# Performance work log

Hardware: AMD Instinct MI355X
Metric: run time of the kernel (lower is better)

## Reference

```python
import jax, jax.numpy as jnp
import numpy as np

B, T, N, D = 8, 512, 64, 128
PRED, HEADS, HID = 96, 8, 256
KERNELS = (17, 49)
NUM_LAYERS = 1
NUM_BLOCKS = 1
IDX_T = np.arange(64)   # lowest 64 of T//2=256 rfft modes (mode_select='low')
IDX_C = np.arange(32)   # min(modes, (N+1)//2)=32 lowest channel-frequency modes


def _mov_avg(x, k):
    # x: [B, T, N]; replicate-pad (k-1)//2 on both ends, then box filter (AvgPool1d stride 1)
    pad = (k - 1) // 2
    xp = jnp.concatenate([jnp.repeat(x[:, :1], pad, axis=1), x, jnp.repeat(x[:, -1:], pad, axis=1)], axis=1)
    c = jnp.cumsum(xp, axis=1)
    c = jnp.concatenate([jnp.zeros_like(c[:, :1]), c], axis=1)
    return (c[:, k:] - c[:, :-k]) / k


def _decomp_multi(x, dec_w, dec_b):
    # series_decomp_multi: softmax-weighted mixture of moving averages
    mm = jnp.stack([_mov_avg(x, k) for k in KERNELS], axis=-1)        # [B,T,N,K]
    w = jax.nn.softmax(x[..., None] * dec_w + dec_b, axis=-1)         # Linear(1,K) on x, softmax over K
    trend = jnp.sum(mm * w, axis=-1)
    return x - trend, trend


def _complex_attn(x, Wq, Wk, Wv, Wo):
    # x: complex64 [B, L, M, D]; multi-head attention over the M selected frequency modes.
    # Real projection weights applied to complex activations; attention weights are
    # softmax over |q k^H| / sqrt(dh); values stay complex.
    Bq, L, M, Dm = x.shape
    dh = Dm // HEADS
    q = jnp.einsum('blmd,de->blme', x, Wq).reshape(Bq, L, M, HEADS, dh)
    k = jnp.einsum('blmd,de->blme', x, Wk).reshape(Bq, L, M, HEADS, dh)
    v = jnp.einsum('blmd,de->blme', x, Wv).reshape(Bq, L, M, HEADS, dh)
    s = jnp.einsum('blmhd,blnhd->blhmn', q, jnp.conj(k))              # complex scores
    w = jax.nn.softmax(jnp.abs(s) / np.sqrt(dh), axis=-1)             # real attn weights
    o = jnp.einsum('blhmn,blnhd->blmhd', w.astype(x.dtype), v).reshape(Bq, L, M, Dm)
    return jnp.einsum('blmd,de->blme', o, Wo)


def _cem(x, Wq, Wk, Wv, Wo):
    # channel-frequency attention; x: [B, N, T, D]
    xp = jnp.transpose(x, (0, 2, 1, 3))                               # [B,T,N,D]
    xf = jnp.fft.rfft(xp, axis=2)                                     # [B,T,N//2+1,D]
    xs = xf[:, :, IDX_C, :]                                           # gather selected modes
    for _ in range(NUM_LAYERS):
        xs = _complex_attn(xs, Wq, Wk, Wv, Wo)
    yf = jnp.zeros((x.shape[0], T, N // 2 + 1, D), dtype=xf.dtype).at[:, :, IDX_C, :].set(xs)
    y = jnp.fft.irfft(yf, n=N, axis=2)
    return jnp.transpose(y, (0, 2, 1, 3))


def _tem(x, Wq, Wk, Wv, Wo):
    # temporal-frequency attention; x: [B, N, T, D]
    xf = jnp.fft.rfft(x, axis=2)                                      # [B,N,T//2+1,D]
    xs = xf[:, :, IDX_T, :]
    for _ in range(NUM_LAYERS):
        xs = _complex_attn(xs, Wq, Wk, Wv, Wo)
    yf = jnp.zeros((x.shape[0], N, T // 2 + 1, D), dtype=xf.dtype).at[:, :, IDX_T, :].set(xs)
    return jnp.fft.irfft(yf, n=T, axis=2)


def setup_inputs() -> dict:
    key = jax.random.key(0)
    ks = jax.random.split(key, 24)
    r = lambda i, shape, s: jax.random.normal(ks[i], shape, jnp.float32) * s
    K = len(KERNELS)
    return {
        'x': jax.random.normal(ks[0], (B, T, N), jnp.float32),
        'embeddings': jax.random.normal(ks[1], (1, D), jnp.float32),
        'dec_w': r(2, (K,), 1.0),
        'dec_b': jnp.zeros((K,), jnp.float32),
        'mlp_w1': r(3, (T, HID), 1.0 / np.sqrt(T)),
        'mlp_b1': jnp.zeros((HID,), jnp.float32),
        'mlp_w2': r(4, (HID, HID), 1.0 / np.sqrt(HID)),
        'mlp_b2': jnp.zeros((HID,), jnp.float32),
        'mlp_w3': r(5, (HID, PRED), 1.0 / np.sqrt(HID)),
        'mlp_b3': jnp.zeros((PRED,), jnp.float32),
        'cem_Wq': r(6, (D, D), 0.02), 'cem_Wk': r(7, (D, D), 0.02),
        'cem_Wv': r(8, (D, D), 0.02), 'cem_Wo': r(9, (D, D), 0.02),
        'tem_Wq': r(10, (D, D), 0.02), 'tem_Wk': r(11, (D, D), 0.02),
        'tem_Wv': r(12, (D, D), 0.02), 'tem_Wo': r(13, (D, D), 0.02),
        'dr_w': r(14, (D, 1), 1.0 / np.sqrt(D)),
        'dr_b': jnp.zeros((1,), jnp.float32),
        'out_w': r(15, (T, PRED), 1.0 / np.sqrt(T)),
        'out_b': jnp.zeros((PRED,), jnp.float32),
        'W_fuse': jnp.ones((2,), jnp.float32),
    }


def reference(x, embeddings, dec_w, dec_b, mlp_w1, mlp_b1, mlp_w2, mlp_b2, mlp_w3, mlp_b3,
              cem_Wq, cem_Wk, cem_Wv, cem_Wo, tem_Wq, tem_Wk, tem_Wv, tem_Wo,
              dr_w, dr_b, out_w, out_b, W_fuse):
    res, trend = _decomp_multi(x, dec_w, dec_b)
    t = jnp.transpose(trend, (0, 2, 1))                               # [B,N,T]
    h = jax.nn.relu(t @ mlp_w1 + mlp_b1)
    h = jax.nn.relu(h @ mlp_w2 + mlp_b2)
    trend_out = jnp.transpose(h @ mlp_w3 + mlp_b3, (0, 2, 1))         # [B,PRED,N]
    # tokenEmb: [B,T,N] -> [B,N,T,1] * [1,D]
    xe = jnp.transpose(res, (0, 2, 1))[..., None] * embeddings[0]      # [B,N,T,D]
    for _ in range(NUM_BLOCKS):
        xe = _cem(xe, cem_Wq, cem_Wk, cem_Wv, cem_Wo)
    for _ in range(NUM_BLOCKS):
        xe = _tem(xe, tem_Wq, tem_Wk, tem_Wv, tem_Wo)
    xr = jnp.einsum('bntd,do->bnto', xe, dr_w)[..., 0] + dr_b[0]      # dim_reduction -> [B,N,T]
    xo = jnp.transpose(jnp.einsum('bnt,tp->bnp', xr, out_w) + out_b, (0, 2, 1))  # [B,PRED,N]
    return W_fuse[0] * xo + W_fuse[1] * trend_out
```

## Files before the change

### kernel.cpp

```cpp
#include <hip/hip_runtime.h>
#include <hip/hip_bf16.h>

typedef __hip_bfloat16 bf16;

constexpr int CB = 8;
constexpr int CT = 512;
constexpr int CN = 64;
constexpr int CD = 128;
constexpr int CP = 96;
constexpr int CH = 8;
constexpr int CDH = 16;
constexpr int CHID = 256;
constexpr int CM = 32;
constexpr int CG = 64;
constexpr float TWO_PI = 6.28318530717958647692f;

__device__ __forceinline__ float LD(const void* p, size_t i, bool f) {
  return f ? ((const float*)p)[i] : __bfloat162float(((const bf16*)p)[i]);
}
template <bool F32>
__device__ __forceinline__ float LDT(const void* p, size_t i) {
  return F32 ? ((const float*)p)[i] : __bfloat162float(((const bf16*)p)[i]);
}

__device__ __forceinline__ bool detect_f32(const void* x) {
  const unsigned int* xw = (const unsigned int*)x;
  unsigned int w = xw[threadIdx.x & 63];
  unsigned int e = (w >> 7) & 0xFF;
  unsigned long long m = __ballot(e >= 0x90 || e <= 0x60);
  return __popcll(m) > 3;
}

__device__ __forceinline__ float2 pkfma(float2 a, float2 b, float2 c) {
  return make_float2(fmaf(a.x, b.x, c.x), fmaf(a.y, b.y, c.y));
}

struct MArgs {
  const void *x, *dec_w, *dec_b, *out_w, *emb, *cWq, *cWk, *cWv, *cWo;
  const void *tWq, *tWk, *tWv, *tWo, *drw, *drb, *out_b, *wfuse;
  const void *w1, *b1, *w2, *b2, *w3, *b3;
  float *trendo, *Pbuf, *ewq, *ewk, *ewv, *wod, *owr, *owi;
  void* out;
};

template <bool F32>
__device__ void k2_body(float* sm, const MArgs& a) {
  float* xbuf = sm;
  float* rows = sm + 2560;
  float* h1 = sm + 4608;
  float* h2 = sm + 5632;
  int r0 = blockIdx.x * 4;
  int b = r0 >> 6, n0 = r0 & 63;
  int tid = threadIdx.x;
  size_t xb = (size_t)b * CT * CN + n0;
  for (int i = tid; i < CT * 4; i += 256) {
    int t = i >> 2, q = i & 3;
    xbuf[t * 5 + q] = LDT<F32>(a.x, xb + (size_t)t * CN + q);
  }
  __syncthreads();
  {
    float w0 = LDT<F32>(a.dec_w, 0), w1 = LDT<F32>(a.dec_w, 1);
    float c0 = LDT<F32>(a.dec_b, 0), c1 = LDT<F32>(a.dec_b, 1);
    int q = tid & 3, tl = tid >> 2;
    int t0 = tl * 8;
    float s17 = 0.f, s49 = 0.f;
    #pragma unroll
    for (int o = -8; o <= 8; ++o) {
      int u = t0 + o; u = u < 0 ? 0 : (u > CT - 1 ? CT - 1 : u);
      s17 += xbuf[u * 5 + q];
    }
    #pragma unroll
    for (int o = -24; o <= 24; ++o) {
      int u = t0 + o; u = u < 0 ? 0 : (u > CT - 1 ? CT - 1 : u);
      s49 += xbuf[u * 5 + q];
    }
    #pragma unroll
    for (int k = 0; k < 8; ++k) {
      int t = t0 + k;
      if (k > 0) {
        int up8 = t + 8 > CT - 1 ? CT - 1 : t + 8;
        int dn9 = t - 9 < 0 ? 0 : t - 9;
        int up24 = t + 24 > CT - 1 ? CT - 1 : t + 24;
        int dn25 = t - 25 < 0 ? 0 : t - 25;
        s17 += xbuf[up8 * 5 + q] - xbuf[dn9 * 5 + q];
        s49 += xbuf[up24 * 5 + q] - xbuf[dn25 * 5 + q];
      }
      float m0 = s17 * (1.f / 17.f), m1 = s49 * (1.f / 49.f);
      float xv = xbuf[t * 5 + q];
      float l0 = xv * w0 + c0, l1 = xv * w1 + c1;
      float mx = fmaxf(l0, l1);
      float e0 = __expf(l0 - mx), e1 = __expf(l1 - mx);
      rows[q * CT + t] = (e0 * m0 + e1 * m1) / (e0 + e1);
    }
  }
  __syncthreads();
  int c = tid;
  float a0, a1, a2, a3;
  {
    float bias = LDT<F32>(a.b1, c);
    a0 = a1 = a2 = a3 = 0.f;
    #pragma unroll 16
    for (int t = 0; t < CT; ++t) {
      float w = LDT<F32>(a.w1, t * CHID + c);
      a0 += rows[0 * CT + t] * w; a1 += rows[1 * CT + t] * w;
      a2 += rows[2 * CT + t] * w; a3 += rows[3 * CT + t] * w;
    }
    h1[0 * CHID + c] = fmaxf(a0 + bias, 0.f); h1[1 * CHID + c] = fmaxf(a1 + bias, 0.f);
    h1[2 * CHID + c] = fmaxf(a2 + bias, 0.f); h1[3 * CHID + c] = fmaxf(a3 + bias, 0.f);
  }
  __syncthreads();
  {
    float bias = LDT<F32>(a.b2, c);
    a0 = a1 = a2 = a3 = 0.f;
    #pragma unroll 16
    for (int i = 0; i < CHID; ++i) {
      float w = LDT<F32>(a.w2, i * CHID + c);
      a0 += h1[0 * CHID + i] * w; a1 += h1[1 * CHID + i] * w;
      a2 += h1[2 * CHID + i] * w; a3 += h1[3 * CHID + i] * w;
    }
    h2[0 * CHID + c] = fmaxf(a0 + bias, 0.f); h2[1 * CHID + c] = fmaxf(a1 + bias, 0.f);
    h2[2 * CHID + c] = fmaxf(a2 + bias, 0.f); h2[3 * CHID + c] = fmaxf(a3 + bias, 0.f);
  }
  __syncthreads();
  if (tid < 2 * CP) {
    int p = tid < CP ? tid : tid - CP;
    int qh = tid < CP ? 0 : 2;
    float bias = LDT<F32>(a.b3, p);
    a0 = a1 = 0.f;
    #pragma unroll 16
    for (int i = 0; i < CHID; ++i) {
      float w = LDT<F32>(a.w3, i * CP + p);
      a0 += h2[qh * CHID + i] * w; a1 += h2[(qh + 1) * CHID + i] * w;
    }
    a.trendo[((size_t)(b * CN + n0 + qh)) * CP + p] = a0 + bias;
    a.trendo[((size_t)(b * CN + n0 + qh + 1)) * CP + p] = a1 + bias;
  }
}

__global__ __launch_bounds__(256, 4) void kS2(MArgs a) {
  __shared__ __align__(16) float sm[6656];
  bool f32 = detect_f32(a.x);
  int blk = blockIdx.x, tid = threadIdx.x;
  if (blk < 128) {
    if (f32) k2_body<true>(sm, a);
    else     k2_body<false>(sm, a);
  } else if (blk < 1152) {
    float* xl = sm;
    float* rowl = sm + 3328;
    float* Rr = sm + 3584;
    float* Ri = sm + 3712;
    float* aR = sm + 3840;
    float* Sr = sm + 3968;
    float* Si = sm + 4992;
    float* chtmp = sm + 6016;
    float* chl = sm + 6144;
    float* eml = sm + 6152;
    int bk = blk - 128;
    int b = bk >> 7, tbase = (bk & 127) * 4;
    int w = tid >> 6, lane = tid & 63;
    size_t xb = (size_t)b * CT * CN;
    for (int i = tid; i < 52 * 64; i += 256) {
      int r = i >> 6, n = i & 63;
      int u = tbase - 24 + r; u = u < 0 ? 0 : (u > CT - 1 ? CT - 1 : u);
      xl[i] = LD(a.x, xb + (size_t)u * CN + n, f32);
    }
    if (tid < 128) eml[tid] = LD(a.emb, tid, f32);
    __syncthreads();
    if (tid < 128) {
      float pq = 0, pk = 0;
      #pragma unroll 8
      for (int d = 0; d < CD; ++d) {
        float em = eml[d];
        pq += em * LD(a.cWq, d * CD + tid, f32);
        pk += em * LD(a.cWk, d * CD + tid, f32);
      }
      chtmp[tid] = pq * pk;
    }
    __syncthreads();
    if (tid < CH) {
      float s = 0;
      #pragma unroll
      for (int j = 0; j < 16; ++j) s += chtmp[tid * 16 + j];
      chl[tid] = fabsf(s);
    }
    {
      int t = tbase + w;
      int Lt = 24 + w;
      float w0 = LD(a.dec_w, 0, f32), w1 = LD(a.dec_w, 1, f32);
      float c0 = LD(a.dec_b, 0, f32), c1 = LD(a.dec_b, 1, f32);
      float s17 = 0;
      #pragma unroll
      for (int o = -8; o <= 8; ++o) s17 += xl[(Lt + o) * 64 + lane];
      float s49 = 0;
      #pragma unroll
      for (int o = -24; o <= 24; ++o) s49 += xl[(Lt + o) * 64 + lane];
      float m0 = s17 * (1.f / 17.f), m1 = s49 * (1.f / 49.f);
      float xv = xl[Lt * 64 + lane];
      float l0 = xv * w0 + c0, l1 = xv * w1 + c1;
      float mx = fmaxf(l0, l1);
      float e0 = __expf(l0 - mx), e1 = __expf(l1 - mx);
      float tr = (e0 * m0 + e1 * m1) / (e0 + e1);
      rowl[w * 64 + lane] = xv - tr;
      (void)t;
    }
    __syncthreads();
    if (lane < CM) {
      float cf, sf;
      sincosf((float)lane * (TWO_PI / CN), &sf, &cf);
      float wr = 1.f, wi = 0.f, rr = 0.f, ri = 0.f;
      #pragma unroll 8
      for (int n2 = 0; n2 < CN; ++n2) {
        float xv = rowl[w * 64 + n2];
        rr = fmaf(xv, wr, rr); ri = fmaf(-xv, wi, ri);
        float nr = wr * cf - wi * sf; wi = wi * cf + wr * sf; wr = nr;
      }
      Rr[w * 32 + lane] = rr; Ri[w * 32 + lane] = ri;
      aR[w * 32 + lane] = sqrtf(rr * rr + ri * ri);
    }
    __syncthreads();
    float amax = 0;
    for (int m = 0; m < CM; ++m) amax = fmaxf(amax, aR[w * 32 + m]);
    #pragma unroll
    for (int i = 0; i < 4; ++i) {
      int pair = lane + 64 * i;
      int h = pair >> 5, m = pair & 31;
      float alpha = 0.25f * chl[h] * aR[w * 32 + m];
      float den = 0, sr = 0, si = 0;
      for (int n2 = 0; n2 < CM; ++n2) {
        float e = __expf(alpha * (aR[w * 32 + n2] - amax));
        den += e; sr += e * Rr[w * 32 + n2]; si += e * Ri[w * 32 + n2];
      }
      Sr[w * 256 + pair] = sr / den; Si[w * 256 + pair] = si / den;
    }
    __syncthreads();
    {
      int n2 = lane, t = tbase + w;
      float acc[8];
      #pragma unroll
      for (int h = 0; h < CH; ++h) acc[h] = Sr[w * 256 + h * 32];
      float cd, sd;
      sincosf((float)n2 * (TWO_PI / CN), &sd, &cd);
      float px = cd, py = sd;
      for (int f = 1; f < CM; ++f) {
        #pragma unroll
        for (int h = 0; h < CH; ++h)
          acc[h] += 2.f * (Sr[w * 256 + h * 32 + f] * px - Si[w * 256 + h * 32 + f] * py);
        float nx = px * cd - py * sd; py = py * cd + px * sd; px = nx;
      }
      float* Pb = a.Pbuf + (((size_t)(b * CN + n2)) * CT + t) * CH;
      ((float4*)Pb)[0] = make_float4(acc[0] * (1.f / CN), acc[1] * (1.f / CN),
                                     acc[2] * (1.f / CN), acc[3] * (1.f / CN));
      ((float4*)Pb)[1] = make_float4(acc[4] * (1.f / CN), acc[5] * (1.f / CN),
                                     acc[6] * (1.f / CN), acc[7] * (1.f / CN));
    }
  } else if (blk < 1216) {
    float* ps = sm;
    int g = blk - 1152;
    int tc = tid >> 7, idx = tid & 127;
    if (idx < CP) {
      int p = idx, t0 = tc * 256;
      float s0, c0v, ss, cs;
      sincosf((float)((g * t0) & (CT - 1)) * (TWO_PI / CT), &s0, &c0v);
      sincosf((float)g * (TWO_PI / CT), &ss, &cs);
      float wr = c0v, wi = s0, ar = 0.f, ai = 0.f;
      #pragma unroll 16
      for (int t = 0; t < 256; ++t) {
        float w = LD(a.out_w, (size_t)(t0 + t) * CP + p, f32);
        ar = fmaf(w, wr, ar); ai = fmaf(w, wi, ai);
        float nr = wr * cs - wi * ss; wi = wi * cs + wr * ss; wr = nr;
      }
      ps[(tc * CP + p) * 2] = ar; ps[(tc * CP + p) * 2 + 1] = ai;
    }
    __syncthreads();
    if (tid < CP) {
      a.owr[g * CP + tid] = ps[tid * 2] + ps[(CP + tid) * 2];
      a.owi[g * CP + tid] = ps[tid * 2 + 1] + ps[(CP + tid) * 2 + 1];
    }
  } else if (blk < 1228) {
    float* eml = sm;
    float* evl = sm + 128;
    float* ewoh = sm + 160;
    int bi = blk - 1216;
    int half = tid >> 7, e = tid & 127;
    int pairIdx = bi * 2 + half;
    int which = pairIdx >> 3, h = pairIdx & 7;
    if (tid < 128) eml[tid] = LD(a.emb, tid, f32);
    __syncthreads();
    if (e < 16) {
      float acc = 0;
      #pragma unroll 8
      for (int d = 0; d < CD; ++d) acc += eml[d] * LD(a.cWv, d * CD + h * CDH + e, f32);
      evl[half * 16 + e] = acc;
    }
    __syncthreads();
    {
      float acc = 0;
      #pragma unroll
      for (int j = 0; j < CDH; ++j)
        acc += evl[half * 16 + j] * LD(a.cWo, (h * CDH + j) * CD + e, f32);
      ewoh[half * 128 + e] = acc;
    }
    __syncthreads();
    {
      const void* W = which == 0 ? a.tWq : (which == 1 ? a.tWk : a.tWv);
      float acc = 0;
      #pragma unroll 8
      for (int d = 0; d < CD; ++d) acc += ewoh[half * 128 + d] * LD(W, d * CD + e, f32);
      (which == 0 ? a.ewq : (which == 1 ? a.ewk : a.ewv))[h * CD + e] = acc;
    }
  } else {
    float* drl = sm;
    if (tid < 128) drl[tid] = LD(a.drw, tid, f32);
    __syncthreads();
    if (tid < 128) {
      float acc = 0;
      #pragma unroll 8
      for (int d = 0; d < CD; ++d) acc += LD(a.tWo, tid * CD + d, f32) * drl[d];
      a.wod[tid] = acc;
    }
  }
}

__global__ __launch_bounds__(256, 4) void kS3(MArgs a) {
  __shared__ __align__(16) float sm[7872];
  float* Pl = sm;
  float* QL = sm + 4096;
  float* Cl = sm + 5120;
  float* Ul = sm + 5632;
  float2* vdL = (float2*)(sm + 5696);
  float2* zL = (float2*)(sm + 6720);
  float* zrow = sm + 7744;
  bool f32 = detect_f32(a.x);
  int blk = blockIdx.x, tid = threadIdx.x;
  int b = blk >> 6, n = blk & 63;
  const float4* Pp4 = (const float4*)(a.Pbuf + ((size_t)(b * CN + n)) * CT * CH);
  float4* Pl4 = (float4*)Pl;
  for (int i = tid; i < CT * CH / 4; i += 256) Pl4[i] = Pp4[i];
  for (int id = tid; id < 512 + 64; id += 256) {
    if (id < 512) {
      int h = id >> 6, aa = (id >> 3) & 7, b2 = id & 7;
      float c = 0;
      #pragma unroll
      for (int j = 0; j < CDH; ++j)
        c += a.ewq[aa * CD + h * CDH + j] * a.ewk[b2 * CD + h * CDH + j];
      Cl[id] = c;
    } else {
      int r = id - 512;
      int h = r >> 3, aa = r & 7;
      float c = 0;
      #pragma unroll
      for (int j = 0; j < CDH; ++j) c += a.ewv[aa * CD + h * CDH + j] * a.wod[h * CDH + j];
      Ul[r] = c;
    }
  }
  __syncthreads();
  {
    int g1 = tid >> 3, h = tid & 7, g2 = g1 + 32;
    float s1, c1, s2, c2;
    sincosf((float)g1 * (TWO_PI / CT), &s1, &c1);
    sincosf((float)g2 * (TWO_PI / CT), &s2, &c2);
    float wr1 = 1.f, wi1 = 0.f, wr2 = 1.f, wi2 = 0.f;
    float r1 = 0, i1 = 0, r2 = 0, i2 = 0;
    #pragma unroll 8
    for (int t = 0; t < CT; ++t) {
      float p = Pl[t * CH + h];
      r1 += p * wr1; i1 += p * wi1;
      r2 += p * wr2; i2 += p * wi2;
      float nr1 = wr1 * c1 + wi1 * s1; wi1 = wi1 * c1 - wr1 * s1; wr1 = nr1;
      float nr2 = wr2 * c2 + wi2 * s2; wi2 = wi2 * c2 - wr2 * s2; wr2 = nr2;
    }
    QL[g1 * 16 + h * 2] = r1; QL[g1 * 16 + h * 2 + 1] = i1;
    QL[g2 * 16 + h * 2] = r2; QL[g2 * 16 + h * 2 + 1] = i2;
  }
  __syncthreads();
  int h0 = tid >> 6, m = tid & 63;
  float2 qp[8];
  {
    const float4* q4 = (const float4*)(QL + m * 16);
    #pragma unroll
    for (int j = 0; j < 4; ++j) {
      float4 y = q4[j];
      qp[2 * j] = make_float2(y.x, y.y);
      qp[2 * j + 1] = make_float2(y.z, y.w);
    }
  }
  #pragma unroll
  for (int e2 = 0; e2 < 2; ++e2) {
    int hh = h0 + e2 * 4;
    float vr = 0, vi = 0;
    #pragma unroll
    for (int aa = 0; aa < 8; ++aa) {
      float u = Ul[hh * 8 + aa];
      vr += qp[aa].x * u; vi += qp[aa].y * u;
    }
    vdL[hh * 64 + m] = make_float2(vr, vi);
  }
  __syncthreads();
  for (int e2 = 0; e2 < 2; ++e2) {
    int hh = h0 + e2 * 4;
    float2 uu[8], vv[8];
    #pragma unroll
    for (int bb = 0; bb < 8; ++bb) {
      float sr = 0, si = 0;
      #pragma unroll
      for (int aa = 0; aa < 8; ++aa) {
        float c = Cl[(hh * 8 + aa) * 8 + bb];
        sr += qp[aa].x * c; si += qp[aa].y * c;
      }
      uu[bb] = make_float2(sr, si);
      vv[bb] = make_float2(si, -sr);
    }
    float mx = -1e30f, den = 0.f, zr = 0.f, zi = 0.f;
    #pragma unroll 4
    for (int g = 0; g < CG; ++g) {
      const float4* k4p = (const float4*)(QL + g * 16);
      float2 sr2 = make_float2(0.f, 0.f), si2 = make_float2(0.f, 0.f);
      #pragma unroll
      for (int j = 0; j < 4; ++j) {
        float4 y = k4p[j];
        float2 y0 = make_float2(y.x, y.y), y1 = make_float2(y.z, y.w);
        sr2 = pkfma(uu[2 * j], y0, sr2); si2 = pkfma(vv[2 * j], y0, si2);
        sr2 = pkfma(uu[2 * j + 1], y1, sr2); si2 = pkfma(vv[2 * j + 1], y1, si2);
      }
      float sr = sr2.x + sr2.y;
      float si = si2.x + si2.y;
      float s = 0.25f * sqrtf(sr * sr + si * si);
      if (s > mx) {
        float f = __expf(mx - s);
        den *= f; zr *= f; zi *= f; mx = s;
      }
      float e = __expf(s - mx);
      float2 vd = vdL[hh * 64 + g];
      den += e; zr += e * vd.x; zi += e * vd.y;
    }
    float rv = 1.f / den;
    zL[hh * 64 + m] = make_float2(zr * rv, zi * rv);
  }
  __syncthreads();
  if (tid < 128) {
    int g = tid >> 1, c = tid & 1;
    float acc = 0;
    #pragma unroll
    for (int hh = 0; hh < CH; ++hh) acc += c ? zL[hh * 64 + g].y : zL[hh * 64 + g].x;
    zrow[g * 2 + c] = acc;
  }
  __syncthreads();
  if (tid < CP) {
    int p = tid;
    float acc = zrow[0] * a.owr[p] - zrow[1] * a.owi[p];
    #pragma unroll 8
    for (int g = 1; g < CG; ++g)
      acc += 2.f * (zrow[g * 2] * a.owr[g * CP + p] - zrow[g * 2 + 1] * a.owi[g * CP + p]);
    float xo = acc * (1.f / CT) + LD(a.drb, 0, f32) * a.owr[p] + LD(a.out_b, p, f32);
    float val = LD(a.wfuse, 0, f32) * xo
              + LD(a.wfuse, 1, f32) * a.trendo[((size_t)(b * CN + n)) * CP + p];
    size_t oidx = ((size_t)(b * CP + p)) * CN + n;
    if (f32) ((float*)a.out)[oidx] = val;
    else ((bf16*)a.out)[oidx] = __float2bfloat16(val);
  }
}

extern "C" void kernel_launch(void* const* d_in, const int* in_sizes, int n_in,
                              void* d_out, int out_size, void* d_ws, size_t ws_size,
                              hipStream_t stream) {
  float* W = (float*)d_ws;
  MArgs a;
  a.x = d_in[0];   a.emb = d_in[1];  a.dec_w = d_in[2]; a.dec_b = d_in[3];
  a.w1 = d_in[4];  a.b1 = d_in[5];   a.w2 = d_in[6];    a.b2 = d_in[7];
  a.w3 = d_in[8];  a.b3 = d_in[9];
  a.cWq = d_in[10]; a.cWk = d_in[11]; a.cWv = d_in[12]; a.cWo = d_in[13];
  a.tWq = d_in[14]; a.tWk = d_in[15]; a.tWv = d_in[16]; a.tWo = d_in[17];
  a.drw = d_in[18]; a.drb = d_in[19]; a.out_w = d_in[20]; a.out_b = d_in[21];
  a.wfuse = d_in[22];
  a.trendo = W; W += (size_t)CB * CN * CP;
  a.Pbuf = W;   W += (size_t)CB * CN * CT * CH;
  a.ewq = W;    W += CH * CD;
  a.ewk = W;    W += CH * CD;
  a.ewv = W;    W += CH * CD;
  a.wod = W;    W += CD;
  a.owr = W;    W += CG * CP;
  a.owi = W;    W += CG * CP;
  a.out = d_out;

  kS2<<<1229, 256, 0, stream>>>(a);
  kS3<<<512, 256, 0, stream>>>(a);
}
```

Before: 210.1 us.

## Reorder separable 2D DFT: time-DFT on frequency modes before channel inverse DFT

The original computed an inverse channel-DFT per time step (64 channels × 512 t × 8 heads) and then a 512-point time DFT per (b,n). This version first stores the 32 selected channel-frequency scores per time step and runs the time DFT on those 32×2 real/imag series in a new kernel. The channel inverse DFT is then applied only to the 64 selected time modes in the final kernel, which shrinks the intermediate buffer and the work per stage. The trend-MLP blocks move into the middle kernel, which adds a third launch plus an extra workspace round trip.

```diff
diff --git a/kernel.cpp b/kernel.cpp
--- a/kernel.cpp
+++ b/kernel.cpp
@@ -39,112 +39,15 @@
   const void *x, *dec_w, *dec_b, *out_w, *emb, *cWq, *cWk, *cWv, *cWo;
   const void *tWq, *tWk, *tWv, *tWo, *drw, *drb, *out_b, *wfuse;
   const void *w1, *b1, *w2, *b2, *w3, *b3;
-  float *trendo, *Pbuf, *ewq, *ewk, *ewv, *wod, *owr, *owi;
+  float *trendo, *Sb, *Shat, *ewq, *ewk, *ewv, *wod, *owr, *owi;
   void* out;
 };
 
-template <bool F32>
-__device__ void k2_body(float* sm, const MArgs& a) {
-  float* xbuf = sm;
-  float* rows = sm + 2560;
-  float* h1 = sm + 4608;
-  float* h2 = sm + 5632;
-  int r0 = blockIdx.x * 4;
-  int b = r0 >> 6, n0 = r0 & 63;
-  int tid = threadIdx.x;
-  size_t xb = (size_t)b * CT * CN + n0;
-  for (int i = tid; i < CT * 4; i += 256) {
-    int t = i >> 2, q = i & 3;
-    xbuf[t * 5 + q] = LDT<F32>(a.x, xb + (size_t)t * CN + q);
-  }
-  __syncthreads();
-  {
-    float w0 = LDT<F32>(a.dec_w, 0), w1 = LDT<F32>(a.dec_w, 1);
-    float c0 = LDT<F32>(a.dec_b, 0), c1 = LDT<F32>(a.dec_b, 1);
-    int q = tid & 3, tl = tid >> 2;
-    int t0 = tl * 8;
-    float s17 = 0.f, s49 = 0.f;
-    #pragma unroll
-    for (int o = -8; o <= 8; ++o) {
-      int u = t0 + o; u = u < 0 ? 0 : (u > CT - 1 ? CT - 1 : u);
-      s17 += xbuf[u * 5 + q];
-    }
-    #pragma unroll
-    for (int o = -24; o <= 24; ++o) {
-      int u = t0 + o; u = u < 0 ? 0 : (u > CT - 1 ? CT - 1 : u);
-      s49 += xbuf[u * 5 + q];
-    }
-    #pragma unroll
-    for (int k = 0; k < 8; ++k) {
-      int t = t0 + k;
-      if (k > 0) {
-        int up8 = t + 8 > CT - 1 ? CT - 1 : t + 8;
-        int dn9 = t - 9 < 0 ? 0 : t - 9;
-        int up24 = t + 24 > CT - 1 ? CT - 1 : t + 24;
-        int dn25 = t - 25 < 0 ? 0 : t - 25;
-        s17 += xbuf[up8 * 5 + q] - xbuf[dn9 * 5 + q];
-        s49 += xbuf[up24 * 5 + q] - xbuf[dn25 * 5 + q];
-      }
-      float m0 = s17 * (1.f / 17.f), m1 = s49 * (1.f / 49.f);
-      float xv = xbuf[t * 5 + q];
-      float l0 = xv * w0 + c0, l1 = xv * w1 + c1;
-      float mx = fmaxf(l0, l1);
-      float e0 = __expf(l0 - mx), e1 = __expf(l1 - mx);
-      rows[q * CT + t] = (e0 * m0 + e1 * m1) / (e0 + e1);
-    }
-  }
-  __syncthreads();
-  int c = tid;
-  float a0, a1, a2, a3;
-  {
-    float bias = LDT<F32>(a.b1, c);
-    a0 = a1 = a2 = a3 = 0.f;
-    #pragma unroll 16
-    for (int t = 0; t < CT; ++t) {
-      float w = LDT<F32>(a.w1, t * CHID + c);
-      a0 += rows[0 * CT + t] * w; a1 += rows[1 * CT + t] * w;
-      a2 += rows[2 * CT + t] * w; a3 += rows[3 * CT + t] * w;
-    }
-    h1[0 * CHID + c] = fmaxf(a0 + bias, 0.f); h1[1 * CHID + c] = fmaxf(a1 + bias, 0.f);
-    h1[2 * CHID + c] = fmaxf(a2 + bias, 0.f); h1[3 * CHID + c] = fmaxf(a3 + bias, 0.f);
-  }
-  __syncthreads();
-  {
-    float bias = LDT<F32>(a.b2, c);
-    a0 = a1 = a2 = a3 = 0.f;
-    #pragma unroll 16
-    for (int i = 0; i < CHID; ++i) {
-      float w = LDT<F32>(a.w2, i * CHID + c);
-      a0 += h1[0 * CHID + i] * w; a1 += h1[1 * CHID + i] * w;
-      a2 += h1[2 * CHID + i] * w; a3 += h1[3 * CHID + i] * w;
-    }
-    h2[0 * CHID + c] = fmaxf(a0 + bias, 0.f); h2[1 * CHID + c] = fmaxf(a1 + bias, 0.f);
-    h2[2 * CHID + c] = fmaxf(a2 + bias, 0.f); h2[3 * CHID + c] = fmaxf(a3 + bias, 0.f);
-  }
-  __syncthreads();
-  if (tid < 2 * CP) {
-    int p = tid < CP ? tid : tid - CP;
-    int qh = tid < CP ? 0 : 2;
-    float bias = LDT<F32>(a.b3, p);
-    a0 = a1 = 0.f;
-    #pragma unroll 16
-    for (int i = 0; i < CHID; ++i) {
-      float w = LDT<F32>(a.w3, i * CP + p);
-      a0 += h2[qh * CHID + i] * w; a1 += h2[(qh + 1) * CHID + i] * w;
-    }
-    a.trendo[((size_t)(b * CN + n0 + qh)) * CP + p] = a0 + bias;
-    a.trendo[((size_t)(b * CN + n0 + qh + 1)) * CP + p] = a1 + bias;
-  }
-}
-
-__global__ __launch_bounds__(256, 4) void kS2(MArgs a) {
+__global__ __launch_bounds__(256, 4) void kA(MArgs a) {
   __shared__ __align__(16) float sm[6656];
   bool f32 = detect_f32(a.x);
   int blk = blockIdx.x, tid = threadIdx.x;
-  if (blk < 128) {
-    if (f32) k2_body<true>(sm, a);
-    else     k2_body<false>(sm, a);
-  } else if (blk < 1152) {
+  if (blk < 1024) {
     float* xl = sm;
     float* rowl = sm + 3328;
     float* Rr = sm + 3584;
@@ -155,8 +58,7 @@
     float* chtmp = sm + 6016;
     float* chl = sm + 6144;
     float* eml = sm + 6152;
-    int bk = blk - 128;
-    int b = bk >> 7, tbase = (bk & 127) * 4;
+    int b = blk >> 7, tbase = (blk & 127) * 4;
     int w = tid >> 6, lane = tid & 63;
     size_t xb = (size_t)b * CT * CN;
     for (int i = tid; i < 52 * 64; i += 256) {
@@ -184,7 +86,6 @@
       chl[tid] = fabsf(s);
     }
     {
-      int t = tbase + w;
       int Lt = 24 + w;
       float w0 = LD(a.dec_w, 0, f32), w1 = LD(a.dec_w, 1, f32);
       float c0 = LD(a.dec_b, 0, f32), c1 = LD(a.dec_b, 1, f32);
@@ -201,7 +102,6 @@
       float e0 = __expf(l0 - mx), e1 = __expf(l1 - mx);
       float tr = (e0 * m0 + e1 * m1) / (e0 + e1);
       rowl[w * 64 + lane] = xv - tr;
-      (void)t;
     }
     __syncthreads();
     if (lane < CM) {
@@ -234,28 +134,16 @@
     }
     __syncthreads();
     {
-      int n2 = lane, t = tbase + w;
-      float acc[8];
-      #pragma unroll
-      for (int h = 0; h < CH; ++h) acc[h] = Sr[w * 256 + h * 32];
-      float cd, sd;
-      sincosf((float)n2 * (TWO_PI / CN), &sd, &cd);
-      float px = cd, py = sd;
-      for (int f = 1; f < CM; ++f) {
-        #pragma unroll
-        for (int h = 0; h < CH; ++h)
-          acc[h] += 2.f * (Sr[w * 256 + h * 32 + f] * px - Si[w * 256 + h * 32 + f] * py);
-        float nx = px * cd - py * sd; py = py * cd + px * sd; px = nx;
-      }
-      float* Pb = a.Pbuf + (((size_t)(b * CN + n2)) * CT + t) * CH;
-      ((float4*)Pb)[0] = make_float4(acc[0] * (1.f / CN), acc[1] * (1.f / CN),
-                                     acc[2] * (1.f / CN), acc[3] * (1.f / CN));
-      ((float4*)Pb)[1] = make_float4(acc[4] * (1.f / CN), acc[5] * (1.f / CN),
-                                     acc[6] * (1.f / CN), acc[7] * (1.f / CN));
-    }
-  } else if (blk < 1216) {
+      int p = tid;
+      float4 vR = make_float4(Sr[p], Sr[256 + p], Sr[512 + p], Sr[768 + p]);
+      float4 vI = make_float4(Si[p], Si[256 + p], Si[512 + p], Si[768 + p]);
+      size_t off = ((size_t)(b * 256 + p)) * 1024 + tbase;
+      *(float4*)(a.Sb + off) = vR;
+      *(float4*)(a.Sb + off + 512) = vI;
+    }
+  } else if (blk < 1088) {
     float* ps = sm;
-    int g = blk - 1152;
+    int g = blk - 1024;
     int tc = tid >> 7, idx = tid & 127;
     if (idx < CP) {
       int p = idx, t0 = tc * 256;
@@ -276,11 +164,11 @@
       a.owr[g * CP + tid] = ps[tid * 2] + ps[(CP + tid) * 2];
       a.owi[g * CP + tid] = ps[tid * 2 + 1] + ps[(CP + tid) * 2 + 1];
     }
-  } else if (blk < 1228) {
+  } else if (blk < 1100) {
     float* eml = sm;
     float* evl = sm + 128;
     float* ewoh = sm + 160;
-    int bi = blk - 1216;
+    int bi = blk - 1088;
     int half = tid >> 7, e = tid & 127;
     int pairIdx = bi * 2 + half;
     int which = pairIdx >> 3, h = pairIdx & 7;
@@ -321,21 +209,141 @@
   }
 }
 
-__global__ __launch_bounds__(256, 4) void kS3(MArgs a) {
-  __shared__ __align__(16) float sm[7872];
-  float* Pl = sm;
-  float* QL = sm + 4096;
-  float* Cl = sm + 5120;
-  float* Ul = sm + 5632;
-  float2* vdL = (float2*)(sm + 5696);
-  float2* zL = (float2*)(sm + 6720);
-  float* zrow = sm + 7744;
+template <bool F32>
+__device__ void k2_body(float* sm, const MArgs& a, int r0) {
+  float* xbuf = sm;
+  float* rows = sm + 2560;
+  float* h1 = sm + 4608;
+  float* h2 = sm + 5632;
+  int b = r0 >> 6, n0 = r0 & 63;
+  int tid = threadIdx.x;
+  size_t xb = (size_t)b * CT * CN + n0;
+  for (int i = tid; i < CT * 4; i += 256) {
+    int t = i >> 2, q = i & 3;
+    xbuf[t * 5 + q] = LDT<F32>(a.x, xb + (size_t)t * CN + q);
+  }
+  __syncthreads();
+  {
+    float w0 = LDT<F32>(a.dec_w, 0), w1 = LDT<F32>(a.dec_w, 1);
+    float c0 = LDT<F32>(a.dec_b, 0), c1 = LDT<F32>(a.dec_b, 1);
+    int q = tid & 3, tl = tid >> 2;
+    int t0 = tl * 8;
+    float s17 = 0.f, s49 = 0.f;
+    #pragma unroll
+    for (int o = -8; o <= 8; ++o) {
+      int u = t0 + o; u = u < 0 ? 0 : (u > CT - 1 ? CT - 1 : u);
+      s17 += xbuf[u * 5 + q];
+    }
+    #pragma unroll
+    for (int o = -24; o <= 24; ++o) {
+      int u = t0 + o; u = u < 0 ? 0 : (u > CT - 1 ? CT - 1 : u);
+      s49 += xbuf[u * 5 + q];
+    }
+    #pragma unroll
+    for (int k = 0; k < 8; ++k) {
+      int t = t0 + k;
+      if (k > 0) {
+        int up8 = t + 8 > CT - 1 ? CT - 1 : t + 8;
+        int dn9 = t - 9 < 0 ? 0 : t - 9;
+        int up24 = t + 24 > CT - 1 ? CT - 1 : t + 24;
+        int dn25 = t - 25 < 0 ? 0 : t - 25;
+        s17 += xbuf[up8 * 5 + q] - xbuf[dn9 * 5 + q];
+        s49 += xbuf[up24 * 5 + q] - xbuf[dn25 * 5 + q];
+      }
+      float m0 = s17 * (1.f / 17.f), m1 = s49 * (1.f / 49.f);
+      float xv = xbuf[t * 5 + q];
+      float l0 = xv * w0 + c0, l1 = xv * w1 + c1;
+      float mx = fmaxf(l0, l1);
+      float e0 = __expf(l0 - mx), e1 = __expf(l1 - mx);
+      rows[q * CT + t] = (e0 * m0 + e1 * m1) / (e0 + e1);
+    }
+  }
+  __syncthreads();
+  int c = tid;
+  float a0, a1, a2, a3;
+  {
+    float bias = LDT<F32>(a.b1, c);
+    a0 = a1 = a2 = a3 = 0.f;
+    #pragma unroll 16
+    for (int t = 0; t < CT; ++t) {
+      float w = LDT<F32>(a.w1, t * CHID + c);
+      a0 += rows[0 * CT + t] * w; a1 += rows[1 * CT + t] * w;
+      a2 += rows[2 * CT + t] * w; a3 += rows[3 * CT + t] * w;
+    }
+    h1[0 * CHID + c] = fmaxf(a0 + bias, 0.f); h1[1 * CHID + c] = fmaxf(a1 + bias, 0.f);
+    h1[2 * CHID + c] = fmaxf(a2 + bias, 0.f); h1[3 * CHID + c] = fmaxf(a3 + bias, 0.f);
+  }
+  __syncthreads();
+  {
+    float bias = LDT<F32>(a.b2, c);
+    a0 = a1 = a2 = a3 = 0.f;
+    #pragma unroll 16
+    for (int i = 0; i < CHID; ++i) {
+      float w = LDT<F32>(a.w2, i * CHID + c);
+      a0 += h1[0 * CHID + i] * w; a1 += h1[1 * CHID + i] * w;
+      a2 += h1[2 * CHID + i] * w; a3 += h1[3 * CHID + i] * w;
+    }
+    h2[0 * CHID + c] = fmaxf(a0 + bias, 0.f); h2[1 * CHID + c] = fmaxf(a1 + bias, 0.f);
+    h2[2 * CHID + c] = fmaxf(a2 + bias, 0.f); h2[3 * CHID + c] = fmaxf(a3 + bias, 0.f);
+  }
+  __syncthreads();
+  if (tid < 2 * CP) {
+    int p = tid < CP ? tid : tid - CP;
+    int qh = tid < CP ? 0 : 2;
+    float bias = LDT<F32>(a.b3, p);
+    a0 = a1 = 0.f;
+    #pragma unroll 16
+    for (int i = 0; i < CHID; ++i) {
+      float w = LDT<F32>(a.w3, i * CP + p);
+      a0 += h2[qh * CHID + i] * w; a1 += h2[(qh + 1) * CHID + i] * w;
+    }
+    a.trendo[((size_t)(b * CN + n0 + qh)) * CP + p] = a0 + bias;
+    a.trendo[((size_t)(b * CN + n0 + qh + 1)) * CP + p] = a1 + bias;
+  }
+}
+
+__global__ __launch_bounds__(256, 4) void kB(MArgs a) {
+  __shared__ __align__(16) float sm[6656];
+  int blk = blockIdx.x, tid = threadIdx.x;
+  if (blk < 1024) {
+    const float4* src = (const float4*)(a.Sb + (size_t)blk * 2048);
+    float4* dst = (float4*)sm;
+    for (int i = tid; i < 512; i += 256) dst[i] = src[i];
+    __syncthreads();
+    int w = tid >> 6, g = tid & 63;
+    int s = blk * 4 + w;
+    int part = s & 1, f = (s >> 1) & 31, h = (s >> 6) & 7, b = s >> 9;
+    float cs, sn;
+    sincosf((float)g * (TWO_PI / CT), &sn, &cs);
+    float wr = 1.f, wi = 0.f, qr = 0.f, qi = 0.f;
+    const float* sq = sm + w * 512;
+    #pragma unroll 8
+    for (int t = 0; t < CT; ++t) {
+      float p = sq[t];
+      qr = fmaf(p, wr, qr); qi = fmaf(p, wi, qi);
+      float nr = wr * cs + wi * sn; wi = wi * cs - wr * sn; wr = nr;
+    }
+    ((float2*)a.Shat)[((size_t)((b * 64 + g) * 8 + h)) * 64 + f * 2 + part] =
+        make_float2(qr, qi);
+  } else {
+    bool f32 = detect_f32(a.x);
+    int r0 = (blk - 1024) * 4;
+    if (f32) k2_body<true>(sm, a, r0);
+    else     k2_body<false>(sm, a, r0);
+  }
+}
+
+__global__ __launch_bounds__(256, 4) void kC(MArgs a) {
+  __shared__ __align__(16) float sm[3840];
+  float* QL = sm;
+  float* Cl = sm + 1024;
+  float* Ul = sm + 1536;
+  float2* vdL = (float2*)(sm + 1600);
+  float2* zL = (float2*)(sm + 2624);
+  float* zrow = sm + 3648;
   bool f32 = detect_f32(a.x);
   int blk = blockIdx.x, tid = threadIdx.x;
   int b = blk >> 6, n = blk & 63;
-  const float4* Pp4 = (const float4*)(a.Pbuf + ((size_t)(b * CN + n)) * CT * CH);
-  float4* Pl4 = (float4*)Pl;
-  for (int i = tid; i < CT * CH / 4; i += 256) Pl4[i] = Pp4[i];
   for (int id = tid; id < 512 + 64; id += 256) {
     if (id < 512) {
       int h = id >> 6, aa = (id >> 3) & 7, b2 = id & 7;
@@ -353,24 +361,27 @@
       Ul[r] = c;
     }
   }
-  __syncthreads();
   {
-    int g1 = tid >> 3, h = tid & 7, g2 = g1 + 32;
-    float s1, c1, s2, c2;
-    sincosf((float)g1 * (TWO_PI / CT), &s1, &c1);
-    sincosf((float)g2 * (TWO_PI / CT), &s2, &c2);
-    float wr1 = 1.f, wi1 = 0.f, wr2 = 1.f, wi2 = 0.f;
-    float r1 = 0, i1 = 0, r2 = 0, i2 = 0;
-    #pragma unroll 8
-    for (int t = 0; t < CT; ++t) {
-      float p = Pl[t * CH + h];
-      r1 += p * wr1; i1 += p * wi1;
-      r2 += p * wr2; i2 += p * wi2;
-      float nr1 = wr1 * c1 + wi1 * s1; wi1 = wi1 * c1 - wr1 * s1; wr1 = nr1;
-      float nr2 = wr2 * c2 + wi2 * s2; wi2 = wi2 * c2 - wr2 * s2; wr2 = nr2;
-    }
-    QL[g1 * 16 + h * 2] = r1; QL[g1 * 16 + h * 2 + 1] = i1;
-    QL[g2 * 16 + h * 2] = r2; QL[g2 * 16 + h * 2 + 1] = i2;
+    float cn, snn;
+    sincosf((float)n * (TWO_PI / CN), &snn, &cn);
+    #pragma unroll
+    for (int e = 0; e < 2; ++e) {
+      int task = tid * 2 + e;
+      int g = task >> 3, h = task & 7;
+      const float4* Sp = (const float4*)(a.Shat + ((size_t)((b * 64 + g) * 8 + h)) * 128);
+      float4 f0 = Sp[0];
+      float qre = 0.5f * f0.x, qim = 0.5f * f0.y;
+      float px = cn, py = snn;
+      #pragma unroll 8
+      for (int f = 1; f < CM; ++f) {
+        float4 ff = Sp[f];
+        qre += ff.x * px - ff.z * py;
+        qim += ff.y * px - ff.w * py;
+        float nx = px * cn - py * snn; py = py * cn + px * snn; px = nx;
+      }
+      QL[g * 16 + h * 2] = qre * (1.f / 32.f);
+      QL[g * 16 + h * 2 + 1] = qim * (1.f / 32.f);
+    }
   }
   __syncthreads();
   int h0 = tid >> 6, m = tid & 63;
@@ -473,7 +484,8 @@
   a.drw = d_in[18]; a.drb = d_in[19]; a.out_w = d_in[20]; a.out_b = d_in[21];
   a.wfuse = d_in[22];
   a.trendo = W; W += (size_t)CB * CN * CP;
-  a.Pbuf = W;   W += (size_t)CB * CN * CT * CH;
+  a.Sb = W;     W += (size_t)CB * CH * CM * 2 * CT;
+  a.Shat = W;   W += (size_t)CB * CG * CH * CM * 4;
   a.ewq = W;    W += CH * CD;
   a.ewk = W;    W += CH * CD;
   a.ewv = W;    W += CH * CD;
@@ -482,6 +494,7 @@
   a.owi = W;    W += CG * CP;
   a.out = d_out;
 
-  kS2<<<1229, 256, 0, stream>>>(a);
-  kS3<<<512, 256, 0, stream>>>(a);
-}
+  kA<<<1101, 256, 0, stream>>>(a);
+  kB<<<1152, 256, 0, stream>>>(a);
+  kC<<<512, 256, 0, stream>>>(a);
+}
```

After: 247.0 us. +17.6%, slower.

## Rewrite temporal DFT as radix-8 split and double threads in attention kernel

Applied to the files above, without the earlier changes.

The second kernel now runs 512 threads per block instead of 256, so each thread handles one head instead of two. The 512-point DFT over time, computed for the 64 low modes, is split into eight strided sub-DFTs followed by an 8-point twiddle combine. That shortens each thread's twiddle recurrence and spreads the work over more threads. The P tile is stored with a padded stride to avoid LDS bank conflicts, and the inner products use native vector float2 types. The risks are higher register pressure from the 8-way accumulators and slightly different rounding in the DFT.

```diff
diff --git a/kernel.cpp b/kernel.cpp
--- a/kernel.cpp
+++ b/kernel.cpp
@@ -2,6 +2,7 @@
 #include <hip/hip_bf16.h>
 
 typedef __hip_bfloat16 bf16;
+typedef float v2f __attribute__((ext_vector_type(2)));
 
 constexpr int CB = 8;
 constexpr int CT = 512;
@@ -29,10 +30,6 @@
   unsigned int e = (w >> 7) & 0xFF;
   unsigned long long m = __ballot(e >= 0x90 || e <= 0x60);
   return __popcll(m) > 3;
-}
-
-__device__ __forceinline__ float2 pkfma(float2 a, float2 b, float2 c) {
-  return make_float2(fmaf(a.x, b.x, c.x), fmaf(a.y, b.y, c.y));
 }
 
 struct MArgs {
@@ -184,7 +181,6 @@
       chl[tid] = fabsf(s);
     }
     {
-      int t = tbase + w;
       int Lt = 24 + w;
       float w0 = LD(a.dec_w, 0, f32), w1 = LD(a.dec_w, 1, f32);
       float c0 = LD(a.dec_b, 0, f32), c1 = LD(a.dec_b, 1, f32);
@@ -201,7 +197,6 @@
       float e0 = __expf(l0 - mx), e1 = __expf(l1 - mx);
       float tr = (e0 * m0 + e1 * m1) / (e0 + e1);
       rowl[w * 64 + lane] = xv - tr;
-      (void)t;
     }
     __syncthreads();
     if (lane < CM) {
@@ -321,22 +316,25 @@
   }
 }
 
-__global__ __launch_bounds__(256, 4) void kS3(MArgs a) {
-  __shared__ __align__(16) float sm[7872];
+__global__ __launch_bounds__(512, 4) void kC(MArgs a) {
+  __shared__ __align__(16) float sm[7904];
   float* Pl = sm;
-  float* QL = sm + 4096;
-  float* Cl = sm + 5120;
-  float* Ul = sm + 5632;
-  float2* vdL = (float2*)(sm + 5696);
-  float2* zL = (float2*)(sm + 6720);
-  float* zrow = sm + 7744;
+  float* QL = sm + 4128;
+  float* Cl = sm + 5152;
+  float* Ul = sm + 5664;
+  float2* vdL = (float2*)(sm + 5728);
+  float2* zL = (float2*)(sm + 6752);
+  float* zrow = sm + 7776;
   bool f32 = detect_f32(a.x);
   int blk = blockIdx.x, tid = threadIdx.x;
   int b = blk >> 6, n = blk & 63;
-  const float4* Pp4 = (const float4*)(a.Pbuf + ((size_t)(b * CN + n)) * CT * CH);
-  float4* Pl4 = (float4*)Pl;
-  for (int i = tid; i < CT * CH / 4; i += 256) Pl4[i] = Pp4[i];
-  for (int id = tid; id < 512 + 64; id += 256) {
+  const float4* src4 = (const float4*)(a.Pbuf + ((size_t)(b * CN + n)) * CT * CH);
+  for (int i = tid; i < 1024; i += 512) {
+    int t = i >> 1, half = i & 1;
+    int k = t >> 6, u = t & 63;
+    *(float4*)(Pl + k * 516 + u * 8 + half * 4) = src4[i];
+  }
+  for (int id = tid; id < 512 + 64; id += 512) {
     if (id < 512) {
       int h = id >> 6, aa = (id >> 3) & 7, b2 = id & 7;
       float c = 0;
@@ -355,86 +353,87 @@
   }
   __syncthreads();
   {
-    int g1 = tid >> 3, h = tid & 7, g2 = g1 + 32;
-    float s1, c1, s2, c2;
-    sincosf((float)g1 * (TWO_PI / CT), &s1, &c1);
-    sincosf((float)g2 * (TWO_PI / CT), &s2, &c2);
-    float wr1 = 1.f, wi1 = 0.f, wr2 = 1.f, wi2 = 0.f;
-    float r1 = 0, i1 = 0, r2 = 0, i2 = 0;
-    #pragma unroll 8
-    for (int t = 0; t < CT; ++t) {
-      float p = Pl[t * CH + h];
-      r1 += p * wr1; i1 += p * wi1;
-      r2 += p * wr2; i2 += p * wi2;
-      float nr1 = wr1 * c1 + wi1 * s1; wi1 = wi1 * c1 - wr1 * s1; wr1 = nr1;
-      float nr2 = wr2 * c2 + wi2 * s2; wi2 = wi2 * c2 - wr2 * s2; wr2 = nr2;
-    }
-    QL[g1 * 16 + h * 2] = r1; QL[g1 * 16 + h * 2 + 1] = i1;
-    QL[g2 * 16 + h * 2] = r2; QL[g2 * 16 + h * 2 + 1] = i2;
-  }
-  __syncthreads();
-  int h0 = tid >> 6, m = tid & 63;
-  float2 qp[8];
-  {
-    const float4* q4 = (const float4*)(QL + m * 16);
-    #pragma unroll
-    for (int j = 0; j < 4; ++j) {
-      float4 y = q4[j];
-      qp[2 * j] = make_float2(y.x, y.y);
-      qp[2 * j + 1] = make_float2(y.z, y.w);
-    }
-  }
+    int g = tid >> 3, h = tid & 7;
+    float cs, sn;
+    sincosf((float)g * (TWO_PI / CT), &sn, &cs);
+    float wr = 1.f, wi = 0.f;
+    float car[8] = {0, 0, 0, 0, 0, 0, 0, 0};
+    float cai[8] = {0, 0, 0, 0, 0, 0, 0, 0};
+    #pragma unroll 4
+    for (int u = 0; u < 64; ++u) {
+      int base = u * 8 + h;
+      #pragma unroll
+      for (int k = 0; k < 8; ++k) {
+        float p = Pl[k * 516 + base];
+        car[k] = fmaf(p, wr, car[k]);
+        cai[k] = fmaf(p, wi, cai[k]);
+      }
+      float nr = wr * cs + wi * sn; wi = wi * cs - wr * sn; wr = nr;
+    }
+    float cs8, sn8;
+    sincosf((float)(g & 7) * (TWO_PI / 8.f), &sn8, &cs8);
+    float pr = 1.f, pi = 0.f, qr = 0.f, qi = 0.f;
+    #pragma unroll
+    for (int k = 0; k < 8; ++k) {
+      qr += car[k] * pr - cai[k] * pi;
+      qi += cai[k] * pr + car[k] * pi;
+      float nr2 = pr * cs8 + pi * sn8; pi = pi * cs8 - pr * sn8; pr = nr2;
+    }
+    QL[g * 16 + h * 2] = qr;
+    QL[g * 16 + h * 2 + 1] = qi;
+  }
+  __syncthreads();
+  int h = tid >> 6, m = tid & 63;
+  v2f qp[8];
+  {
+    const v2f* qrow = (const v2f*)(QL + m * 16);
+    #pragma unroll
+    for (int j = 0; j < 8; ++j) qp[j] = qrow[j];
+  }
+  {
+    float vr = 0, vi = 0;
+    #pragma unroll
+    for (int aa = 0; aa < 8; ++aa) {
+      float u = Ul[h * 8 + aa];
+      vr = fmaf(qp[aa].x, u, vr); vi = fmaf(qp[aa].y, u, vi);
+    }
+    vdL[h * 64 + m] = make_float2(vr, vi);
+  }
+  v2f uu[8], vv[8];
   #pragma unroll
-  for (int e2 = 0; e2 < 2; ++e2) {
-    int hh = h0 + e2 * 4;
-    float vr = 0, vi = 0;
-    #pragma unroll
-    for (int aa = 0; aa < 8; ++aa) {
-      float u = Ul[hh * 8 + aa];
-      vr += qp[aa].x * u; vi += qp[aa].y * u;
-    }
-    vdL[hh * 64 + m] = make_float2(vr, vi);
-  }
-  __syncthreads();
-  for (int e2 = 0; e2 < 2; ++e2) {
-    int hh = h0 + e2 * 4;
-    float2 uu[8], vv[8];
-    #pragma unroll
-    for (int bb = 0; bb < 8; ++bb) {
-      float sr = 0, si = 0;
-      #pragma unroll
-      for (int aa = 0; aa < 8; ++aa) {
-        float c = Cl[(hh * 8 + aa) * 8 + bb];
-        sr += qp[aa].x * c; si += qp[aa].y * c;
-      }
-      uu[bb] = make_float2(sr, si);
-      vv[bb] = make_float2(si, -sr);
-    }
-    float mx = -1e30f, den = 0.f, zr = 0.f, zi = 0.f;
-    #pragma unroll 4
-    for (int g = 0; g < CG; ++g) {
-      const float4* k4p = (const float4*)(QL + g * 16);
-      float2 sr2 = make_float2(0.f, 0.f), si2 = make_float2(0.f, 0.f);
-      #pragma unroll
-      for (int j = 0; j < 4; ++j) {
-        float4 y = k4p[j];
-        float2 y0 = make_float2(y.x, y.y), y1 = make_float2(y.z, y.w);
-        sr2 = pkfma(uu[2 * j], y0, sr2); si2 = pkfma(vv[2 * j], y0, si2);
-        sr2 = pkfma(uu[2 * j + 1], y1, sr2); si2 = pkfma(vv[2 * j + 1], y1, si2);
-      }
-      float sr = sr2.x + sr2.y;
-      float si = si2.x + si2.y;
-      float s = 0.25f * sqrtf(sr * sr + si * si);
-      if (s > mx) {
-        float f = __expf(mx - s);
-        den *= f; zr *= f; zi *= f; mx = s;
-      }
-      float e = __expf(s - mx);
-      float2 vd = vdL[hh * 64 + g];
-      den += e; zr += e * vd.x; zi += e * vd.y;
-    }
+  for (int bb = 0; bb < 8; ++bb) {
+    v2f acc = {0.f, 0.f};
+    #pragma unroll
+    for (int aa = 0; aa < 8; ++aa) acc += qp[aa] * Cl[(h * 8 + aa) * 8 + bb];
+    uu[bb] = acc;
+    vv[bb] = (v2f){acc.y, -acc.x};
+  }
+  __syncthreads();
+  float mx = -1e30f, den = 0.f, zr = 0.f, zi = 0.f;
+  #pragma unroll 4
+  for (int g = 0; g < CG; ++g) {
+    const v2f* y = (const v2f*)(QL + g * 16);
+    v2f sr2 = {0.f, 0.f}, si2 = {0.f, 0.f};
+    #pragma unroll
+    for (int j = 0; j < 8; ++j) {
+      v2f yj = y[j];
+      sr2 = uu[j] * yj + sr2;
+      si2 = vv[j] * yj + si2;
+    }
+    float sr = sr2.x + sr2.y;
+    float si = si2.x + si2.y;
+    float s = 0.25f * sqrtf(sr * sr + si * si);
+    if (s > mx) {
+      float f = __expf(mx - s);
+      den *= f; zr *= f; zi *= f; mx = s;
+    }
+    float e = __expf(s - mx);
+    float2 vd = vdL[h * 64 + g];
+    den += e; zr += e * vd.x; zi += e * vd.y;
+  }
+  {
     float rv = 1.f / den;
-    zL[hh * 64 + m] = make_float2(zr * rv, zi * rv);
+    zL[h * 64 + m] = make_float2(zr * rv, zi * rv);
   }
   __syncthreads();
   if (tid < 128) {
@@ -483,5 +482,5 @@
   a.out = d_out;
 
   kS2<<<1229, 256, 0, stream>>>(a);
-  kS3<<<512, 256, 0, stream>>>(a);
-}
+  kC<<<512, 512, 0, stream>>>(a);
+}
```

Measured after the change: 191.3 us. -8.9%, faster.
